# Kernel tuning notes

Hardware: AMD Instinct MI355X
Metric: run time of the kernel (lower is better)

## Reference

```python
import jax, jax.numpy as jnp
import numpy as np

BETA = 0.9       # leak factor (snn.Leaky beta)
THRESH = 1.0     # default snn.Leaky threshold
ALPHA = 2.0      # default ATan surrogate alpha

@jax.custom_vjp
def atan_spike(x):
    # Heaviside forward, ATan surrogate backward (snntorch default spike_grad)
    return (x > 0).astype(x.dtype)

def _atan_fwd(x):
    return (x > 0).astype(x.dtype), x

def _atan_bwd(x, g):
    # d/dx ~ (alpha/2) / (1 + (pi/2 * alpha * x)^2)
    return (g * (ALPHA / 2) / (1 + (jnp.pi / 2 * ALPHA * x) ** 2),)

atan_spike.defvjp(_atan_fwd, _atan_bwd)

def setup_inputs() -> dict:
    key = jax.random.key(0)
    k1, k2 = jax.random.split(key)
    B, IN, OUT, T = 64, 1024, 1024, 256
    x = jax.random.normal(k1, (B, IN, T), dtype=jnp.float32)
    W = jax.random.normal(k2, (OUT, IN), dtype=jnp.float32) * (1.0 / np.sqrt(IN))
    return {"x": x, "W": W}

def reference(x, W):
    # Batch all per-timestep GEMMs into one contraction: syn[b,o,t]
    syn = jnp.einsum('bit,oi->bot', x, W)
    syn_t = jnp.moveaxis(syn, -1, 0)  # [T, B, OUT]
    mem0 = jnp.zeros(syn.shape[:-1], syn.dtype)  # [B, OUT]

    def step(mem, s):
        # snntorch Leaky (subtract reset): reset from previous mem (detached),
        # then state update, then spike from new mem.
        reset = jax.lax.stop_gradient((mem > THRESH).astype(mem.dtype))
        mem = BETA * mem + s - reset * THRESH
        spk = atan_spike(mem - THRESH)
        return mem, spk

    _, spks = jax.lax.scan(step, mem0, syn_t)  # spks: [T, B, OUT]
    return jnp.moveaxis(spks, 0, -1)  # [B, OUT, T]
```

## Files before the change

### kernel.cpp

```cpp
#include <hip/hip_runtime.h>


#define B_DIM 64
#define IN_DIM 1024
#define OUT_DIM 1024
#define T_DIM 256

typedef int v4i __attribute__((ext_vector_type(4)));
typedef int v16i __attribute__((ext_vector_type(16)));
typedef double v4d __attribute__((ext_vector_type(4)));

#define LO_OFF   0ull
#define WSL_OFF  67108864ull
#define XSL_OFF  73400320ull
#define AL_OFF   174063616ull
#define BE_OFF   174067712ull
#define PART_OFF 174133248ull
#define WS_NEED  175181824ull

__device__ __forceinline__ void gload_lds16(const void* g, void* l)
{
    __builtin_amdgcn_global_load_lds(
        (const __attribute__((address_space(1))) void*)g,
        (__attribute__((address_space(3))) void*)l, 16, 0, 0);
}

__device__ __forceinline__ void dig4_extract(unsigned bits, int bem,
                                             signed char* d )
{
    const int be = (bits >> 23) & 255;
    unsigned M = (bits & 0x7fffffu) | (be ? 0x800000u : 0u);
    const int sh = be - bem + 4;
    unsigned fix = 0;
    if (sh >= 0) fix = M << sh;
    else if (sh > -32) fix = M >> (-sh);
    int d0 = (fix >> 21) & 127, d1 = (fix >> 14) & 127,
        d2 = (fix >> 7) & 127,  d3 = fix & 127;
    if (bits & 0x80000000u) { d0 = -d0; d1 = -d1; d2 = -d2; d3 = -d3; }
    d[0] = (signed char)d0; d[1] = (signed char)d1;
    d[2] = (signed char)d2; d[3] = (signed char)d3;
}

__global__ __launch_bounds__(256) void k_aux_wx(
    const float* __restrict__ W, signed char* __restrict__ wsl,
    int* __restrict__ alpha_e,
    const float* __restrict__ x, float* __restrict__ part)
{
    __shared__ float red[256];
    __shared__ float wrow[1024];
    __shared__ int se;
    __shared__ float4 bp[4][64];
    const int tid = threadIdx.x;

    if (blockIdx.x < 1024) {
        const int o = blockIdx.x;
        float4 v = *(const float4*)&W[(size_t)o * IN_DIM + tid * 4];
        *(float4*)&wrow[tid * 4] = v;
        float m = fmaxf(fmaxf(fabsf(v.x), fabsf(v.y)), fmaxf(fabsf(v.z), fabsf(v.w)));
        red[tid] = m; __syncthreads();
        for (int s = 128; s > 0; s >>= 1) {
            if (tid < s) red[tid] = fmaxf(red[tid], red[tid + s]);
            __syncthreads();
        }
        if (tid == 0) { int e = 0; if (red[0] > 0.f) frexpf(red[0], &e); se = e; alpha_e[o] = e; }
        __syncthreads();
        if (tid >= 64) return;
        const int bem = se + 126;
        const int ks = tid >> 1, khalf = tid & 1;
        const int k0 = tid * 16;
        const int lane = (o & 31) + 32 * khalf;

        signed char dig[16][4];
        #pragma unroll
        for (int j = 0; j < 16; ++j)
            dig4_extract(__float_as_uint(wrow[k0 + j]), bem, dig[j]);

        #pragma unroll
        for (int p = 0; p < 4; ++p) {
            int w[4];
            #pragma unroll
            for (int g = 0; g < 4; ++g)
                w[g] = (dig[4*g][p] & 0xff) | ((dig[4*g+1][p] & 0xff) << 8) |
                       ((dig[4*g+2][p] & 0xff) << 16) | ((dig[4*g+3][p] & 0xff) << 24);
            const size_t base =
                (((size_t)p * 32 + (o >> 5)) * 32 + ks) * 1024 + lane * 16;
            *(v4i*)&wsl[base] = (v4i){w[0], w[1], w[2], w[3]};
        }
    } else {
        const int idx = blockIdx.x - 1024;
        const int ic = idx & 15, b = idx >> 4;
        const int quarter = tid >> 6, t4 = (tid & 63) * 4;
        const float* p = x + ((size_t)b * IN_DIM + ic * 64 + quarter * 16) * T_DIM + t4;
        float4 m4 = make_float4(0.f, 0.f, 0.f, 0.f);
        #pragma unroll
        for (int r = 0; r < 16; ++r) {
            float4 v = *(const float4*)&p[(size_t)r * T_DIM];
            m4.x = fmaxf(m4.x, fabsf(v.x)); m4.y = fmaxf(m4.y, fabsf(v.y));
            m4.z = fmaxf(m4.z, fabsf(v.z)); m4.w = fmaxf(m4.w, fabsf(v.w));
        }
        bp[quarter][tid & 63] = m4;
        __syncthreads();
        if (tid < 64) {
            float4 a = bp[0][tid], b4 = bp[1][tid], c = bp[2][tid], d = bp[3][tid];
            float4 r;
            r.x = fmaxf(fmaxf(a.x, b4.x), fmaxf(c.x, d.x));
            r.y = fmaxf(fmaxf(a.y, b4.y), fmaxf(c.y, d.y));
            r.z = fmaxf(fmaxf(a.z, b4.z), fmaxf(c.z, d.z));
            r.w = fmaxf(fmaxf(a.w, b4.w), fmaxf(c.w, d.w));
            *(float4*)&part[((size_t)b * 16 + ic) * T_DIM + tid * 4] = r;
        }
    }
}

__global__ __launch_bounds__(256) void k_slice_x(const float* __restrict__ x,
    const float* __restrict__ part, int* __restrict__ beta_e,
    signed char* __restrict__ xsl)
{
    __shared__ float ft[64][68];
    __shared__ int se_arr[64];
    const int tb = blockIdx.x;
    const int ib = blockIdx.y;
    const int b  = blockIdx.z;
    const int tid = threadIdx.x;
    const int t0 = tb * 64, i0 = ib * 64;
    #pragma unroll
    for (int p = 0; p < 4; ++p) {
        int id4 = tid + p * 256;
        int il = id4 >> 4, c4 = (id4 & 15) * 4;
        float4 v = *(const float4*)&x[((size_t)b * IN_DIM + i0 + il) * T_DIM + t0 + c4];
        *(float4*)&ft[il][c4] = v;
    }
    if (tid < 64) {
        const int t = t0 + tid;
        float m = 0.f;
        #pragma unroll
        for (int ic = 0; ic < 16; ++ic)
            m = fmaxf(m, part[((size_t)b * 16 + ic) * T_DIM + t]);
        int e = 0;
        if (m > 0.f) frexpf(m, &e);
        se_arr[tid] = e;
        if (ib == 0) beta_e[b * T_DIM + t] = e;
    }
    __syncthreads();

    const int t32l = tid >> 7;
    const int ksl  = (tid >> 6) & 1;
    const int lane = tid & 63;
    const int t_local = t32l * 32 + (lane & 31);
    const int k_local = ksl * 32 + (lane >> 5) * 16;
    const int bem = se_arr[t_local] + 126;

    signed char dig[16][4];
    #pragma unroll
    for (int j = 0; j < 16; ++j)
        dig4_extract(__float_as_uint(ft[k_local + j][t_local]), bem, dig[j]);

    #pragma unroll
    for (int p = 0; p < 4; ++p) {
        int w[4];
        #pragma unroll
        for (int g = 0; g < 4; ++g)
            w[g] = (dig[4*g][p] & 0xff) | ((dig[4*g+1][p] & 0xff) << 8) |
                   ((dig[4*g+2][p] & 0xff) << 16) | ((dig[4*g+3][p] & 0xff) << 24);
        const size_t base =
            ((((size_t)p * B_DIM + b) * 8 + (tb * 2 + t32l)) * 32 + (ib * 2 + ksl)) * 1024
            + lane * 16;
        *(v4i*)&xsl[base] = (v4i){w[0], w[1], w[2], w[3]};
    }
}

#define OZ_LOADS(PF)                                                        \
    {                                                                       \
        _Pragma("unroll")                                                   \
        for (int j = 0; j < 5; ++j) {                                       \
            gload_lds16(gp[j], &LB[PF][lbase + j * 8192]);                  \
            gp[j] += 1024;                                                  \
        }                                                                   \
    }

#define OZ_MATH(CUR)                                                        \
    {                                                                       \
        const signed char* base_ = LB[CUR];                                 \
        v4i af[4];                                                          \
        _Pragma("unroll")                                                   \
        for (int p = 0; p < 4; ++p)                                         \
            af[p] = *(const v4i*)(base_ + p * 2048 + aoffm);                \
        __builtin_amdgcn_s_setprio(1);                                      \
        _Pragma("unroll")                                                   \
        for (int q = 0; q < 4; ++q) {                                       \
            v4i b0 = *(const v4i*)(base_ + q * 8192 + boffm);               \
            v4i b1 = *(const v4i*)(base_ + q * 8192 + boffm + 1024);        \
            _Pragma("unroll")                                               \
            for (int p = 0; p + q < 4; ++p) {                               \
                accA[p + q] = __builtin_amdgcn_mfma_i32_32x32x32_i8(        \
                    af[p], b0, accA[p + q], 0, 0, 0);                       \
                accB[p + q] = __builtin_amdgcn_mfma_i32_32x32x32_i8(        \
                    af[p], b1, accB[p + q], 0, 0, 0);                       \
            }                                                               \
        }                                                                   \
        __builtin_amdgcn_s_setprio(0);                                      \
    }

#define VMBAR(N)                                                            \
    do {                                                                    \
        asm volatile("s_waitcnt vmcnt(" #N ")" ::: "memory");               \
        __builtin_amdgcn_s_barrier();                                       \
    } while (0)

__global__ __launch_bounds__(512, 2) void k_oz_gemm_fused(
    const signed char* __restrict__ wsl, const signed char* __restrict__ xsl,
    const int* __restrict__ alpha_e, const int* __restrict__ beta_e,
    float* __restrict__ out)
{
    __shared__ __align__(16) signed char LB[3][40960];

    const int tid = threadIdx.x;
    const int lane = tid & 63, wave = tid >> 6;
    const int bid = blockIdx.x;
    const int ob = bid >> 6;
    const int rr = bid & 63;
    const int b  = ((rr & 7) << 3) + (rr >> 3);
    const int o0 = ob * 64;
    const int woh = wave >> 2;
    const int wtq = wave & 3;
    const int l16 = lane * 16;

    v16i accA[4], accB[4];
    #pragma unroll
    for (int s = 0; s < 4; ++s) {
        accA[s] = (v16i){0,0,0,0,0,0,0,0,0,0,0,0,0,0,0,0};
        accB[s] = (v16i){0,0,0,0,0,0,0,0,0,0,0,0,0,0,0,0};
    }

    const signed char* gp[5];
    #pragma unroll
    for (int j = 0; j < 5; ++j) {
        const int s = 8 * j + wave;
        if (s < 8) {
            gp[j] = wsl + ((size_t)(s >> 1) << 20)
                        + ((size_t)(2 * ob + (s & 1)) << 15) + l16;
        } else {
            const int u = s - 8;
            gp[j] = xsl + ((size_t)(u >> 3) << 24) + ((size_t)b << 18)
                        + ((size_t)(u & 7) << 15) + l16;
        }
    }
    const int lbase = wave * 1024;

    const int aoffm = woh * 1024 + l16;
    const int boffm = 8192 + wtq * 2048 + l16;

    OZ_LOADS(0)
    OZ_LOADS(1)
    VMBAR(5);

    #pragma unroll 1
    for (int it = 0; it < 10; ++it) {
        OZ_LOADS(2) OZ_MATH(0) VMBAR(5);
        OZ_LOADS(0) OZ_MATH(1) VMBAR(5);
        OZ_LOADS(1) OZ_MATH(2) VMBAR(5);
    }
    OZ_MATH(0) VMBAR(0);
    OZ_MATH(1)

    const int lr = lane & 31;
    const int rv = (lr + 1) * 0x01010101;
    const v4i pav  = {rv, rv, rv, rv};
    const v4i onev = {0x01010101, 0x01010101, 0x01010101, 0x01010101};
    const v16i z = (v16i){0,0,0,0,0,0,0,0,0,0,0,0,0,0,0,0};
    v16i d1 = __builtin_amdgcn_mfma_i32_32x32x32_i8(pav, onev, z, 0, 0, 0);
    v16i d2 = __builtin_amdgcn_mfma_i32_32x32x32_i8(onev, pav, z, 0, 0, 0);

    const int col = (d2[0] >> 5) - 1;
    const int gtA = wtq * 64 + col;
    const int gtB = gtA + 32;
    const int ebA = beta_e[b * T_DIM + gtA];
    const int ebB = beta_e[b * T_DIM + gtB];

    const double C0 = 0x1p-14, C1 = 0x1p-21, C2 = 0x1p-28, C3 = 0x1p-35;
    double synA_[16], synB_[16];
    int go_[16];
    #pragma unroll
    for (int r = 0; r < 16; ++r) {
        const int row = (d1[r] >> 5) - 1;
        const int go = woh * 32 + row;
        go_[r] = go;
        const int ea = alpha_e[o0 + go];
        double vA = (double)accA[0][r] * C0 + (double)accA[1][r] * C1 +
                    (double)accA[2][r] * C2 + (double)accA[3][r] * C3;
        double vB = (double)accB[0][r] * C0 + (double)accB[1][r] * C1 +
                    (double)accB[2][r] * C2 + (double)accB[3][r] * C3;
        synA_[r] = ldexp(vA, ea + ebA);
        synB_[r] = ldexp(vB, ea + ebB);
    }

    double* synbuf = (double*)&LB[0][0];
    float*  spkbuf = (float*)&LB[1][0];
    float*  outp = out + ((size_t)b * OUT_DIM + o0) * T_DIM;
    double mem = 0.0;

    __syncthreads();
    #pragma unroll 1
    for (int c = 0; c < 4; ++c) {
        if (wtq == c) {
            #pragma unroll
            for (int r = 0; r < 16; ++r) {
                synbuf[(size_t)col * 65 + go_[r]]        = synA_[r];
                synbuf[(size_t)(col + 32) * 65 + go_[r]] = synB_[r];
            }
        }
        __syncthreads();
        if (wave == 0) {
            float sp[64];
            #pragma unroll
            for (int g = 0; g < 4; ++g) {
                double sv[16];
                #pragma unroll
                for (int k = 0; k < 16; ++k)
                    sv[k] = synbuf[(size_t)(g * 16 + k) * 65 + lane];
                #pragma unroll
                for (int k = 0; k < 16; ++k) {
                    double a = 0.9 * mem + sv[k];
                    mem = (mem > 1.0) ? (a - 1.0) : a;
                    sp[g * 16 + k] = (mem > 1.0) ? 1.0f : 0.0f;
                }
            }
            #pragma unroll
            for (int k4 = 0; k4 < 16; ++k4)
                *(float4*)&spkbuf[lane * 68 + k4 * 4] = make_float4(
                    sp[k4 * 4], sp[k4 * 4 + 1], sp[k4 * 4 + 2], sp[k4 * 4 + 3]);
        }
        __syncthreads();
        {
            const int o = tid >> 3, tg = tid & 7;
            float4 v0 = *(float4*)&spkbuf[o * 68 + tg * 8];
            float4 v1 = *(float4*)&spkbuf[o * 68 + tg * 8 + 4];
            float* dst = outp + (size_t)o * T_DIM + c * 64 + tg * 8;
            *(float4*)&dst[0] = v0;
            *(float4*)&dst[4] = v1;
        }
        __syncthreads();
    }
}

#define BM 128
#define BN 128
#define BK 16
#define LDA 130

__global__ __launch_bounds__(256, 2) void spk_gemm_mfma64p_kernel(
    const float* __restrict__ x, const float* __restrict__ W,
    float* __restrict__ syn_hi, float* __restrict__ syn_lo)
{
    const int tid  = threadIdx.x;
    const int lane = tid & 63;
    const int wave = tid >> 6;
    const int tb = blockIdx.x, ob = blockIdx.y, b = blockIdx.z;

    __shared__ __align__(16) double As[BK][LDA];
    __shared__ __align__(16) double Bs[BK][LDA];

    const v4d zz = {0.0, 0.0, 0.0, 0.0};
    v4d d1 = __builtin_amdgcn_mfma_f64_16x16x4f64((double)lane, 1.0, zz, 0, 0, 0);
    v4d d2 = __builtin_amdgcn_mfma_f64_16x16x4f64(1.0, (double)lane, zz, 0, 0, 0);
    const bool a_h1 = (((int)d1[0] & 3) == 0);
    const bool b_h1 = (((int)d2[0] & 3) == 0);
    int drow[4];
    #pragma unroll
    for (int r = 0; r < 4; ++r) {
        const int v = (int)d1[r];
        drow[r] = (a_h1 ? (v - 96) >> 2 : (v - 6) >> 4) & 15;
    }
    const int am = a_h1 ? (lane & 15) : (lane >> 2);
    const int ak = a_h1 ? (lane >> 4) : (lane & 3);
    const int bn = b_h1 ? (lane & 15) : (lane >> 2);
    const int bk = b_h1 ? (lane >> 4) : (lane & 3);
    const int dcol = lane & 15;

    const int o0 = ob * BM, t0 = tb * BN;
    const float* Wp = W + (size_t)o0 * IN_DIM;
    const float* xp = x + (size_t)b * IN_DIM * T_DIM + t0;
    const int wo = (wave >> 1) * 64, wt = (wave & 1) * 64;

    v4d acc[4][4];
    #pragma unroll
    for (int i = 0; i < 4; ++i)
        #pragma unroll
        for (int j = 0; j < 4; ++j) acc[i][j] = zz;

    const int ar0 = tid / 4, ac = (tid % 4) * 4;
    const int bkr0 = tid / 32, btc = (tid % 32) * 4;

    float4 pa[2], pb[2];
    #pragma unroll
    for (int p = 0; p < 2; ++p) {
        pa[p] = *(const float4*)&Wp[(size_t)(ar0 + p * 64) * IN_DIM + ac];
        pb[p] = *(const float4*)&xp[(size_t)(bkr0 + p * 8) * T_DIM + btc];
    }

    for (int k0 = 0; k0 < IN_DIM; k0 += BK) {
        #pragma unroll
        for (int p = 0; p < 2; ++p) {
            const int r = ar0 + p * 64;
            As[ac + 0][r] = (double)pa[p].x; As[ac + 1][r] = (double)pa[p].y;
            As[ac + 2][r] = (double)pa[p].z; As[ac + 3][r] = (double)pa[p].w;
            const int kr = bkr0 + p * 8;
            Bs[kr][btc + 0] = (double)pb[p].x; Bs[kr][btc + 1] = (double)pb[p].y;
            Bs[kr][btc + 2] = (double)pb[p].z; Bs[kr][btc + 3] = (double)pb[p].w;
        }
        if (k0 + BK < IN_DIM) {
            #pragma unroll
            for (int p = 0; p < 2; ++p) {
                pa[p] = *(const float4*)&Wp[(size_t)(ar0 + p * 64) * IN_DIM + k0 + BK + ac];
                pb[p] = *(const float4*)&xp[(size_t)(bkr0 + p * 8 + k0 + BK) * T_DIM + btc];
            }
        }
        __syncthreads();
        #pragma unroll
        for (int kk = 0; kk < 4; ++kk) {
            const int kra = kk * 4 + ak, krb = kk * 4 + bk;
            double a[4], bb[4];
            #pragma unroll
            for (int i = 0; i < 4; ++i) a[i] = As[kra][wo + i * 16 + am];
            #pragma unroll
            for (int j = 0; j < 4; ++j) bb[j] = Bs[krb][wt + j * 16 + bn];
            #pragma unroll
            for (int i = 0; i < 4; ++i)
                #pragma unroll
                for (int j = 0; j < 4; ++j)
                    acc[i][j] = __builtin_amdgcn_mfma_f64_16x16x4f64(a[i], bb[j], acc[i][j], 0, 0, 0);
        }
        __syncthreads();
    }

    float* ohi = syn_hi + ((size_t)b * OUT_DIM + o0) * T_DIM + t0;
    float* olo = syn_lo + ((size_t)b * OUT_DIM + o0) * T_DIM + t0;
    #pragma unroll
    for (int i = 0; i < 4; ++i)
        #pragma unroll
        for (int j = 0; j < 4; ++j) {
            const int col = wt + j * 16 + dcol;
            #pragma unroll
            for (int r = 0; r < 4; ++r) {
                double s = acc[i][j][r];
                float hi = (float)s;
                float lo = (float)(s - (double)hi);
                const size_t off = (size_t)(wo + i * 16 + drow[r]) * T_DIM + col;
                ohi[off] = hi; olo[off] = lo;
            }
        }
}

__global__ __launch_bounds__(256) void spk_scan_f64_kernel(
    float* __restrict__ hi, const float* __restrict__ lo)
{
    const int TC = 16;
    __shared__ float thi[256][TC + 1];
    __shared__ float tlo[256][TC + 1];
    const int tid = threadIdx.x;
    const size_t row0 = (size_t)blockIdx.x * 256;

    double mem = 0.0;
    for (int t0 = 0; t0 < T_DIM; t0 += TC) {
        #pragma unroll
        for (int p = 0; p < 4; ++p) {
            int id = tid + p * 256;
            int r = id / 4, c = (id % 4) * 4;
            size_t g = (row0 + r) * T_DIM + t0 + c;
            float4 vh = *(const float4*)&hi[g];
            thi[r][c] = vh.x; thi[r][c+1] = vh.y; thi[r][c+2] = vh.z; thi[r][c+3] = vh.w;
            float4 vl = *(const float4*)&lo[g];
            tlo[r][c] = vl.x; tlo[r][c+1] = vl.y; tlo[r][c+2] = vl.z; tlo[r][c+3] = vl.w;
        }
        __syncthreads();
        float spk[TC];
        #pragma unroll
        for (int t = 0; t < TC; ++t) {
            double s = (double)thi[tid][t] + (double)tlo[tid][t];
            double reset = (mem > 1.0) ? 1.0 : 0.0;
            mem = 0.9 * mem + s - reset;
            spk[t] = ((mem - 1.0) > 0.0) ? 1.0f : 0.0f;
        }
        __syncthreads();
        #pragma unroll
        for (int t = 0; t < TC; ++t) thi[tid][t] = spk[t];
        __syncthreads();
        #pragma unroll
        for (int p = 0; p < 4; ++p) {
            int id = tid + p * 256;
            int r = id / 4, c = (id % 4) * 4;
            float4 v = make_float4(thi[r][c], thi[r][c+1], thi[r][c+2], thi[r][c+3]);
            *(float4*)&hi[(row0 + r) * T_DIM + t0 + c] = v;
        }
        __syncthreads();
    }
}

extern "C" void kernel_launch(void* const* d_in, const int* in_sizes, int n_in,
                              void* d_out, int out_size, void* d_ws, size_t ws_size,
                              hipStream_t stream)
{
    const float* x = (const float*)d_in[0];
    const float* W = (const float*)d_in[1];
    float* hi = (float*)d_out;
    char* ws = (char*)d_ws;
    float* lo = (float*)(ws + LO_OFF);

    if (ws_size >= WS_NEED) {
        signed char* wsl = (signed char*)(ws + WSL_OFF);
        signed char* xsl = (signed char*)(ws + XSL_OFF);
        int* alpha = (int*)(ws + AL_OFF);
        int* beta  = (int*)(ws + BE_OFF);
        float* part = (float*)(ws + PART_OFF);

        k_aux_wx<<<dim3(2048), dim3(256), 0, stream>>>(W, wsl, alpha, x, part);
        k_slice_x<<<dim3(4, 16, B_DIM), dim3(256), 0, stream>>>(x, part, beta, xsl);
        k_oz_gemm_fused<<<dim3(1024), dim3(512), 0, stream>>>(wsl, xsl, alpha, beta, hi);
    } else {
        spk_gemm_mfma64p_kernel<<<dim3(2, 8, B_DIM), dim3(256), 0, stream>>>(x, W, hi, lo);
        spk_scan_f64_kernel<<<dim3((B_DIM * OUT_DIM) / 256), dim3(256), 0, stream>>>(hi, lo);
    }
}
```

Baseline: 310.9 us.

## Fuse x max-reduction and x slicing into single prep kernel

Merges the x column-max pass and the x digit-slicing kernel into one kernel, so each (batch, time-block) block first computes its per-timestep exponents and then slices all 16 input chunks itself. The W slicing moves into the same launch. This removes one kernel launch and the intermediate partial-max buffer round trip through global memory. In exchange, only 256 blocks handle x, each looping over 8 iterations with 512 threads, and x is read twice per block, so there is less parallelism for that part.

```diff
diff --git a/kernel.cpp b/kernel.cpp
--- a/kernel.cpp
+++ b/kernel.cpp
@@ -41,23 +41,111 @@
     d[2] = (signed char)d2; d[3] = (signed char)d3;
 }
 
-__global__ __launch_bounds__(256) void k_aux_wx(
+__global__ __launch_bounds__(512) void k_prep(
     const float* __restrict__ W, signed char* __restrict__ wsl,
     int* __restrict__ alpha_e,
-    const float* __restrict__ x, float* __restrict__ part)
+    const float* __restrict__ x, int* __restrict__ beta_e,
+    signed char* __restrict__ xsl)
 {
     __shared__ float red[256];
     __shared__ float wrow[1024];
     __shared__ int se;
-    __shared__ float4 bp[4][64];
+    __shared__ float ft[2][64][68];
+    __shared__ float4 p1red[32][16];
+    __shared__ float cmax[64];
+    __shared__ int se_arr[64];
     const int tid = threadIdx.x;
 
-    if (blockIdx.x < 1024) {
-        const int o = blockIdx.x;
-        float4 v = *(const float4*)&W[(size_t)o * IN_DIM + tid * 4];
-        *(float4*)&wrow[tid * 4] = v;
-        float m = fmaxf(fmaxf(fabsf(v.x), fabsf(v.y)), fmaxf(fabsf(v.z), fabsf(v.w)));
-        red[tid] = m; __syncthreads();
+    if (blockIdx.x < 256) {
+        const int idx = blockIdx.x;
+        const int tb = idx >> 6;
+        const int b  = idx & 63;
+        const int t0 = tb * 64;
+
+        {
+            const int i_lane = tid >> 4;
+            const int tg = tid & 15;
+            float4 m4 = make_float4(0.f, 0.f, 0.f, 0.f);
+            #pragma unroll 4
+            for (int ic = 0; ic < 32; ++ic) {
+                const int i = ic * 32 + i_lane;
+                float4 v = *(const float4*)&x[((size_t)b * IN_DIM + i) * T_DIM + t0 + tg * 4];
+                m4.x = fmaxf(m4.x, fabsf(v.x)); m4.y = fmaxf(m4.y, fabsf(v.y));
+                m4.z = fmaxf(m4.z, fabsf(v.z)); m4.w = fmaxf(m4.w, fabsf(v.w));
+            }
+            p1red[i_lane][tg] = m4;
+            __syncthreads();
+            if (tid < 16) {
+                float4 r = p1red[0][tid];
+                #pragma unroll 8
+                for (int il = 1; il < 32; ++il) {
+                    float4 v = p1red[il][tid];
+                    r.x = fmaxf(r.x, v.x); r.y = fmaxf(r.y, v.y);
+                    r.z = fmaxf(r.z, v.z); r.w = fmaxf(r.w, v.w);
+                }
+                cmax[tid * 4 + 0] = r.x; cmax[tid * 4 + 1] = r.y;
+                cmax[tid * 4 + 2] = r.z; cmax[tid * 4 + 3] = r.w;
+            }
+            __syncthreads();
+            if (tid < 64) {
+                float m = cmax[tid];
+                int e = 0;
+                if (m > 0.f) frexpf(m, &e);
+                se_arr[tid] = e;
+                beta_e[b * T_DIM + t0 + tid] = e;
+            }
+            __syncthreads();
+        }
+
+        const int half = tid >> 8;
+        const int ttid = tid & 255;
+        const int t32l = ttid >> 7;
+        const int ksl  = (ttid >> 6) & 1;
+        const int lane = ttid & 63;
+        const int t_local = t32l * 32 + (lane & 31);
+        const int k_local = ksl * 32 + (lane >> 5) * 16;
+        const int bem = se_arr[t_local] + 126;
+
+        #pragma unroll 1
+        for (int it2 = 0; it2 < 8; ++it2) {
+            const int ib = it2 * 2 + half;
+            #pragma unroll
+            for (int p = 0; p < 4; ++p) {
+                int id4 = ttid + p * 256;
+                int il = id4 >> 4, c4 = (id4 & 15) * 4;
+                float4 v = *(const float4*)&x[((size_t)b * IN_DIM + ib * 64 + il) * T_DIM + t0 + c4];
+                *(float4*)&ft[half][il][c4] = v;
+            }
+            __syncthreads();
+
+            signed char dig[16][4];
+            #pragma unroll
+            for (int j = 0; j < 16; ++j)
+                dig4_extract(__float_as_uint(ft[half][k_local + j][t_local]), bem, dig[j]);
+
+            #pragma unroll
+            for (int p = 0; p < 4; ++p) {
+                int w[4];
+                #pragma unroll
+                for (int g = 0; g < 4; ++g)
+                    w[g] = (dig[4*g][p] & 0xff) | ((dig[4*g+1][p] & 0xff) << 8) |
+                           ((dig[4*g+2][p] & 0xff) << 16) | ((dig[4*g+3][p] & 0xff) << 24);
+                const size_t base =
+                    ((((size_t)p * B_DIM + b) * 8 + (tb * 2 + t32l)) * 32 + (ib * 2 + ksl)) * 1024
+                    + lane * 16;
+                *(v4i*)&xsl[base] = (v4i){w[0], w[1], w[2], w[3]};
+            }
+            __syncthreads();
+        }
+    } else {
+        const int o = blockIdx.x - 256;
+        if (tid < 256) {
+            float4 v = *(const float4*)&W[(size_t)o * IN_DIM + tid * 4];
+            *(float4*)&wrow[tid * 4] = v;
+            float m = fmaxf(fmaxf(fabsf(v.x), fabsf(v.y)), fmaxf(fabsf(v.z), fabsf(v.w)));
+            red[tid] = m;
+        }
+        __syncthreads();
         for (int s = 128; s > 0; s >>= 1) {
             if (tid < s) red[tid] = fmaxf(red[tid], red[tid + s]);
             __syncthreads();
@@ -86,86 +174,6 @@
                 (((size_t)p * 32 + (o >> 5)) * 32 + ks) * 1024 + lane * 16;
             *(v4i*)&wsl[base] = (v4i){w[0], w[1], w[2], w[3]};
         }
-    } else {
-        const int idx = blockIdx.x - 1024;
-        const int ic = idx & 15, b = idx >> 4;
-        const int quarter = tid >> 6, t4 = (tid & 63) * 4;
-        const float* p = x + ((size_t)b * IN_DIM + ic * 64 + quarter * 16) * T_DIM + t4;
-        float4 m4 = make_float4(0.f, 0.f, 0.f, 0.f);
-        #pragma unroll
-        for (int r = 0; r < 16; ++r) {
-            float4 v = *(const float4*)&p[(size_t)r * T_DIM];
-            m4.x = fmaxf(m4.x, fabsf(v.x)); m4.y = fmaxf(m4.y, fabsf(v.y));
-            m4.z = fmaxf(m4.z, fabsf(v.z)); m4.w = fmaxf(m4.w, fabsf(v.w));
-        }
-        bp[quarter][tid & 63] = m4;
-        __syncthreads();
-        if (tid < 64) {
-            float4 a = bp[0][tid], b4 = bp[1][tid], c = bp[2][tid], d = bp[3][tid];
-            float4 r;
-            r.x = fmaxf(fmaxf(a.x, b4.x), fmaxf(c.x, d.x));
-            r.y = fmaxf(fmaxf(a.y, b4.y), fmaxf(c.y, d.y));
-            r.z = fmaxf(fmaxf(a.z, b4.z), fmaxf(c.z, d.z));
-            r.w = fmaxf(fmaxf(a.w, b4.w), fmaxf(c.w, d.w));
-            *(float4*)&part[((size_t)b * 16 + ic) * T_DIM + tid * 4] = r;
-        }
-    }
-}
-
-__global__ __launch_bounds__(256) void k_slice_x(const float* __restrict__ x,
-    const float* __restrict__ part, int* __restrict__ beta_e,
-    signed char* __restrict__ xsl)
-{
-    __shared__ float ft[64][68];
-    __shared__ int se_arr[64];
-    const int tb = blockIdx.x;
-    const int ib = blockIdx.y;
-    const int b  = blockIdx.z;
-    const int tid = threadIdx.x;
-    const int t0 = tb * 64, i0 = ib * 64;
-    #pragma unroll
-    for (int p = 0; p < 4; ++p) {
-        int id4 = tid + p * 256;
-        int il = id4 >> 4, c4 = (id4 & 15) * 4;
-        float4 v = *(const float4*)&x[((size_t)b * IN_DIM + i0 + il) * T_DIM + t0 + c4];
-        *(float4*)&ft[il][c4] = v;
-    }
-    if (tid < 64) {
-        const int t = t0 + tid;
-        float m = 0.f;
-        #pragma unroll
-        for (int ic = 0; ic < 16; ++ic)
-            m = fmaxf(m, part[((size_t)b * 16 + ic) * T_DIM + t]);
-        int e = 0;
-        if (m > 0.f) frexpf(m, &e);
-        se_arr[tid] = e;
-        if (ib == 0) beta_e[b * T_DIM + t] = e;
-    }
-    __syncthreads();
-
-    const int t32l = tid >> 7;
-    const int ksl  = (tid >> 6) & 1;
-    const int lane = tid & 63;
-    const int t_local = t32l * 32 + (lane & 31);
-    const int k_local = ksl * 32 + (lane >> 5) * 16;
-    const int bem = se_arr[t_local] + 126;
-
-    signed char dig[16][4];
-    #pragma unroll
-    for (int j = 0; j < 16; ++j)
-        dig4_extract(__float_as_uint(ft[k_local + j][t_local]), bem, dig[j]);
-
-    #pragma unroll
-    for (int p = 0; p < 4; ++p) {
-        int w[4];
-        #pragma unroll
-        for (int g = 0; g < 4; ++g)
-            w[g] = (dig[4*g][p] & 0xff) | ((dig[4*g+1][p] & 0xff) << 8) |
-                   ((dig[4*g+2][p] & 0xff) << 16) | ((dig[4*g+3][p] & 0xff) << 24);
-        const size_t base =
-            ((((size_t)p * B_DIM + b) * 8 + (tb * 2 + t32l)) * 32 + (ib * 2 + ksl)) * 1024
-            + lane * 16;
-        *(v4i*)&xsl[base] = (v4i){w[0], w[1], w[2], w[3]};
     }
 }
 
@@ -511,10 +519,8 @@
         signed char* xsl = (signed char*)(ws + XSL_OFF);
         int* alpha = (int*)(ws + AL_OFF);
         int* beta  = (int*)(ws + BE_OFF);
-        float* part = (float*)(ws + PART_OFF);
-
-        k_aux_wx<<<dim3(2048), dim3(256), 0, stream>>>(W, wsl, alpha, x, part);
-        k_slice_x<<<dim3(4, 16, B_DIM), dim3(256), 0, stream>>>(x, part, beta, xsl);
+
+        k_prep<<<dim3(1280), dim3(512), 0, stream>>>(W, wsl, alpha, x, beta, xsl);
         k_oz_gemm_fused<<<dim3(1024), dim3(512), 0, stream>>>(wsl, xsl, alpha, beta, hi);
     } else {
         spk_gemm_mfma64p_kernel<<<dim3(2, 8, B_DIM), dim3(256), 0, stream>>>(x, W, hi, lo);
```

Measured after the change: 319.5 us. 2.8% more time.
